# Performance work log

Hardware: AMD Instinct MI355X
Metric: run time of the kernel (lower is better)

## Reference

```python
import jax, jax.numpy as jnp
import numpy as np

B = 32768
NUM_DENSE = 13
PAD_DENSE = 16  # 13 padded up to multiple of 8
T = 26          # number of categorical tables
V = 100000      # cardinality per table
E = 128         # embedding_dim
BOTTOM_DIMS = [512, 256, 128]
TOP_DIMS = [1024, 1024, 512, 256, 1]
N_FEAT = T + 1  # 27 feature vectors entering interaction
PAIR = N_FEAT * (N_FEAT - 1) // 2  # 351
TOP_IN = PAIR + E   # 479
TOP_PAD = 480       # padded to multiple of 8


def _glorot(key, fan_in, fan_out):
    s = np.sqrt(2.0 / (fan_in + fan_out))
    return jax.random.normal(key, (fan_in, fan_out), jnp.float32) * s


def setup_inputs() -> dict:
    key = jax.random.key(0)
    ks = jax.random.split(key, 32)
    inp = {
        "numerical": jax.random.normal(ks[0], (B, NUM_DENSE), jnp.float32),
        "cat_features": jax.random.randint(ks[1], (B, T), 0, V, jnp.int32),
        "emb_tables": jax.random.normal(ks[2], (T, V, E), jnp.float32) * 0.01,
    }
    # bottom MLP: 16 -> 512 -> 256 -> 128 (all relu)
    d_in = PAD_DENSE
    for i, d in enumerate(BOTTOM_DIMS):
        inp[f"bw{i}"] = _glorot(ks[3 + 2 * i], d_in, d)
        inp[f"bb{i}"] = jax.random.normal(ks[4 + 2 * i], (d,), jnp.float32) * np.sqrt(1.0 / d)
        d_in = d
    # top MLP: 480 -> 1024 -> 1024 -> 512 -> 256 -> 1 (relu except last)
    d_in = TOP_PAD
    for i, d in enumerate(TOP_DIMS):
        inp[f"tw{i}"] = _glorot(ks[12 + 2 * i], d_in, d)
        inp[f"tb{i}"] = jax.random.normal(ks[13 + 2 * i], (d,), jnp.float32) * np.sqrt(1.0 / d)
        d_in = d
    return inp


def reference(numerical, cat_features, emb_tables,
              bw0, bb0, bw1, bb1, bw2, bb2,
              tw0, tb0, tw1, tb1, tw2, tb2, tw3, tb3, tw4, tb4):
    b = numerical.shape[0]
    # --- bottom MLP (dense features padded with zeros to 16) ---
    x = jnp.pad(numerical, ((0, 0), (0, PAD_DENSE - NUM_DENSE)))
    for w, bias in ((bw0, bb0), (bw1, bb1), (bw2, bb2)):
        x = jax.nn.relu(x @ w + bias)
    bottom_out = x  # [B, E]
    # --- multi-table embedding gather: emb_tables[t][cat[:, t]] ---
    emb_out = jax.vmap(lambda tab, idx: tab[idx], in_axes=(0, 1), out_axes=1)(
        emb_tables, cat_features)  # [B, T, E]
    # --- dot interaction ---
    feats = jnp.concatenate([bottom_out[:, None, :], emb_out], axis=1)  # [B, 27, E]
    Z = jnp.einsum('bnd,bmd->bnm', feats, feats)  # [B, 27, 27]
    iu, ju = jnp.triu_indices(N_FEAT, k=1)
    pair = Z[:, iu, ju]  # [B, 351]
    x = jnp.concatenate(
        [bottom_out, pair, jnp.zeros((b, TOP_PAD - TOP_IN), feats.dtype)], axis=1)  # [B, 480]
    # --- top MLP (relu except last layer) ---
    tops = ((tw0, tb0), (tw1, tb1), (tw2, tb2), (tw3, tb3), (tw4, tb4))
    for i, (w, bias) in enumerate(tops):
        x = x @ w + bias
        if i < len(tops) - 1:
            x = jax.nn.relu(x)
    return x  # [B, 1] logits
```

## Files before the change

kernel.cpp:

```cpp
#include <hip/hip_runtime.h>

typedef __bf16 bf16;
typedef __bf16 bf16x4 __attribute__((ext_vector_type(4)));
typedef __bf16 bf16x8 __attribute__((ext_vector_type(8)));
typedef float f32x4 __attribute__((ext_vector_type(4)));

#define B_SZ 32768
#define T_CAT 26
#define V_SZ 100000
#define E_SZ 128

__device__ __forceinline__ void gload_lds16(const void* g, void* l) {
    __builtin_amdgcn_global_load_lds(
        (const __attribute__((address_space(1))) void*)g,
        (__attribute__((address_space(3))) void*)l, 16, 0, 0);
}

struct CJob { const float* W; bf16* Wt; int K, N, Kp, blk0, tk; };
struct CJobs { CJob j[7]; };

__global__ __launch_bounds__(256) void convw_all(CJobs js) {
    __shared__ bf16 tile[64][66];
    const int b = blockIdx.x;
    int ji = 0;
#pragma unroll
    for (int k = 1; k < 7; ++k)
        if (b >= js.j[k].blk0) ji = k;
    const CJob J = js.j[ji];
    const int local = b - J.blk0;
    const int tn = local / J.tk;
    const int tkk = local - tn * J.tk;

    const int t = threadIdx.x;
    const int lx = t & 63;
    const int gy = t >> 6;

#pragma unroll
    for (int kk = 0; kk < 16; ++kk) {
        const int k = tkk * 64 + kk * 4 + gy;
        const int n = tn * 64 + lx;
        const float v = (k < J.K) ? J.W[(long)k * J.N + n] : 0.0f;
        tile[lx][kk * 4 + gy] = (bf16)v;
    }
    __syncthreads();
#pragma unroll
    for (int nn = 0; nn < 16; ++nn) {
        const int nloc = nn * 4 + gy;
        const int n = tn * 64 + nloc;
        const int k = tkk * 64 + lx;
        J.Wt[(long)n * J.Kp + k] = tile[nloc][lx];
    }
}

__global__ __launch_bounds__(256) void make_xpad(const float* __restrict__ num,
                                                 bf16* __restrict__ xp) {
    const int idx = blockIdx.x * 256 + threadIdx.x;
    const int b = idx >> 6, c = idx & 63;
    xp[idx] = (bf16)((c < 13) ? num[(long)b * 13 + c] : 0.0f);
}

template <int RELU>
__global__ __launch_bounds__(256) void gemm_bt(const bf16* __restrict__ A,
                                               const bf16* __restrict__ Bt,
                                               const float* __restrict__ bias,
                                               bf16* __restrict__ C,
                                               int M, int N, int K) {
    __shared__ __align__(16) bf16 As[128 * 64];
    __shared__ __align__(16) bf16 Bs[128 * 64];
    const int t = threadIdx.x;
    const int lane = t & 63;
    const int w = t >> 6;
    const int wm = w >> 1, wn = w & 1;
    const long row0 = (long)blockIdx.y * 128;
    const long col0 = (long)blockIdx.x * 128;

    const int srow = t >> 3;
    const int scol = (t & 7) * 8;
    const bf16* Ag = A + (row0 + srow) * (long)K + scol;
    const bf16* Bg = Bt + (col0 + srow) * (long)K + scol;
    bf16* AsB = &As[w * 512];
    bf16* BsB = &Bs[w * 512];

    f32x4 acc[4][4] = {};

    for (int k0 = 0; k0 < K; k0 += 64) {
#pragma unroll
        for (int q = 0; q < 4; ++q) {
            gload_lds16(Ag + (long)q * 32 * K + k0, AsB + q * 2048);
            gload_lds16(Bg + (long)q * 32 * K + k0, BsB + q * 2048);
        }
        __syncthreads();
#pragma unroll
        for (int s = 0; s < 2; ++s) {
            bf16x8 af[4], bv[4];
#pragma unroll
            for (int i = 0; i < 4; ++i)
                af[i] = *(const bf16x8*)&As[(wm * 64 + i * 16 + (lane & 15)) * 64 +
                                            s * 32 + (lane >> 4) * 8];
#pragma unroll
            for (int j = 0; j < 4; ++j)
                bv[j] = *(const bf16x8*)&Bs[(wn * 64 + j * 16 + (lane & 15)) * 64 +
                                            s * 32 + (lane >> 4) * 8];
#pragma unroll
            for (int i = 0; i < 4; ++i)
#pragma unroll
                for (int j = 0; j < 4; ++j)
                    acc[i][j] = __builtin_amdgcn_mfma_f32_16x16x32_bf16(
                        af[i], bv[j], acc[i][j], 0, 0, 0);
        }
        __syncthreads();
    }

    const int r4 = (lane >> 4) * 4;
    const int cn = lane & 15;
#pragma unroll
    for (int j = 0; j < 4; ++j) {
        const long col = col0 + wn * 64 + j * 16 + cn;
        const float bj = bias[col];
#pragma unroll
        for (int i = 0; i < 4; ++i) {
#pragma unroll
            for (int r = 0; r < 4; ++r) {
                const long row = row0 + wm * 64 + i * 16 + r4 + r;
                float v = acc[i][j][r] + bj;
                if (RELU) v = v > 0.0f ? v : 0.0f;
                C[row * (long)N + col] = (bf16)v;
            }
        }
    }
}

template <int RELU>
__global__ __launch_bounds__(512, 2) void gemm256(const bf16* __restrict__ A,
                                                  const bf16* __restrict__ Bt,
                                                  const float* __restrict__ bias,
                                                  bf16* __restrict__ C,
                                                  int M, int N, int K, int nbx) {
    __shared__ __align__(16) bf16 lds[65536];
    const int t = threadIdx.x;
    const int lane = t & 63;
    const int w = t >> 6;
    const int wm = w >> 2, wn = w & 3;

    const int nwg = gridDim.x;
    const int qch = nwg >> 3;
    const int swz = ((int)blockIdx.x & 7) * qch + ((int)blockIdx.x >> 3);
    const int bx = swz % nbx, by = swz / nbx;
    const long row0 = (long)by * 256;
    const long col0 = (long)bx * 256;

    const int NT = K >> 6;

    const int srow = t >> 2;
    const int scol = (t & 3) * 8;
    const bf16* Ag = A + (row0 + srow) * (long)K + scol;
    const bf16* Bg = Bt + (col0 + srow) * (long)K + scol;

#define STG(BUF, MAT, KH, KT)                                              \
    do {                                                                   \
        const bf16* _g = ((MAT) ? Bg : Ag) + (long)(KT)*64 + (KH)*32;      \
        bf16* _l = &lds[(BUF)*32768 + (MAT)*16384 + (KH)*8192 + w * 512];  \
        gload_lds16(_g, _l);                                               \
        gload_lds16(_g + 128 * (long)K, _l + 4096);                        \
    } while (0)

    const int cm = lane & 15;
    const int kc = lane >> 4;
    const int abase = (wm * 128 + cm) * 32 + kc * 8;
    const int bbase = 16384 + (wn * 64 + cm) * 32 + kc * 8;

    bf16x8 bfr[4];
    f32x4 acc[8][4] = {};

#define PH(BUFB, S, IH, LOADB, STAGE, WAIT)                                   \
    do {                                                                      \
        if (LOADB) {                                                          \
            _Pragma("unroll") for (int j = 0; j < 4; ++j)                     \
                bfr[j] = *(const bf16x8*)&lds[(BUFB) + bbase + (S)*8192 + j*512]; \
        }                                                                     \
        bf16x8 af[4];                                                         \
        _Pragma("unroll") for (int i = 0; i < 4; ++i)                         \
            af[i] = *(const bf16x8*)&lds[(BUFB) + abase + (S)*8192 + ((IH)*4+i)*512]; \
        STAGE;                                                                \
        WAIT;                                                                 \
        asm volatile("" ::: "memory");                                       \
        __builtin_amdgcn_s_barrier();                                        \
        asm volatile("s_waitcnt lgkmcnt(0)" ::: "memory");                    \
        __builtin_amdgcn_s_setprio(1);                                       \
        _Pragma("unroll") for (int i = 0; i < 4; ++i)                         \
            _Pragma("unroll") for (int j = 0; j < 4; ++j)                     \
                acc[(IH)*4 + i][j] = __builtin_amdgcn_mfma_f32_16x16x32_bf16( \
                    af[i], bfr[j], acc[(IH)*4 + i][j], 0, 0, 0);              \
        __builtin_amdgcn_s_setprio(0);                                       \
        asm volatile("" ::: "memory");                                       \
        __builtin_amdgcn_s_barrier();                                        \
        asm volatile("" ::: "memory");                                       \
    } while (0)

#define TILE(BUFB, S1, S2, S3, S4, W4)          \
    PH(BUFB, 0, 0, 1, S1, ((void)0));           \
    PH(BUFB, 0, 1, 0, S2, ((void)0));           \
    PH(BUFB, 1, 0, 1, S3, ((void)0));           \
    PH(BUFB, 1, 1, 0, S4, W4)

#define VM6 asm volatile("s_waitcnt vmcnt(6)" ::: "memory")
#define VM0 asm volatile("s_waitcnt vmcnt(0)" ::: "memory")
#define NOP ((void)0)

    STG(0, 1, 0, 0); STG(0, 0, 0, 0); STG(0, 1, 1, 0); STG(0, 0, 1, 0);
    STG(1, 1, 0, 1); STG(1, 0, 0, 1); STG(1, 1, 1, 1);
    VM6;
    __builtin_amdgcn_s_barrier();

    for (int tt = 0; tt + 3 < NT; tt += 2) {
        TILE(0,
             STG(1, 0, 1, tt + 1),
             STG(0, 1, 0, tt + 2),
             STG(0, 0, 0, tt + 2),
             STG(0, 1, 1, tt + 2),
             VM6);
        TILE(32768,
             STG(0, 0, 1, tt + 2),
             STG(1, 1, 0, tt + 3),
             STG(1, 0, 0, tt + 3),
             STG(1, 1, 1, tt + 3),
             VM6);
    }
    TILE(0, STG(1, 0, 1, NT - 1), NOP, NOP, NOP, VM0);
    TILE(32768, NOP, NOP, NOP, NOP, NOP);

#undef STG
#undef PH
#undef TILE
#undef VM6
#undef VM0
#undef NOP

    const int r4 = kc * 4;
#pragma unroll
    for (int j = 0; j < 4; ++j) {
        const long col = col0 + wn * 64 + j * 16 + cm;
        const float bj = bias[col];
#pragma unroll
        for (int i = 0; i < 8; ++i) {
#pragma unroll
            for (int r = 0; r < 4; ++r) {
                const long row = row0 + wm * 128 + i * 16 + r4 + r;
                float v = acc[i][j][r] + bj;
                if (RELU) v = v > 0.0f ? v : 0.0f;
                C[row * (long)N + col] = (bf16)v;
            }
        }
    }
}

__global__ __launch_bounds__(256) void interact_k(const float* __restrict__ emb,
                                                  const int* __restrict__ cat,
                                                  const bf16* __restrict__ bottom,
                                                  bf16* __restrict__ top_in) {
    __shared__ float gram[4][32 * 32];
    __shared__ __align__(16) bf16 rowbuf[4][512];
    const int t = threadIdx.x;
    const int lane = t & 63;
    const int w = t >> 6;
    const long s = (long)blockIdx.x * 4 + w;

    const int rl = lane & 15;
    const int kg = lane >> 4;

    bf16x8 f[2][4];
#pragma unroll
    for (int i = 0; i < 2; ++i) {
        const int r = i * 16 + rl;
        const float* rowp = nullptr;
        if (r >= 1 && r <= 26) {
            const int idx = cat[s * T_CAT + (r - 1)];
            rowp = emb + ((long)(r - 1) * V_SZ + idx) * E_SZ;
        }
#pragma unroll
        for (int ks = 0; ks < 4; ++ks) {
            const int c = ks * 32 + kg * 8;
            bf16x8 v = {};
            if (r == 0) {
                v = *(const bf16x8*)(bottom + s * 128 + c);
            } else if (r <= 26) {
                const float4 v0 = *(const float4*)(rowp + c);
                const float4 v1 = *(const float4*)(rowp + c + 4);
                v[0]=(bf16)v0.x; v[1]=(bf16)v0.y; v[2]=(bf16)v0.z; v[3]=(bf16)v0.w;
                v[4]=(bf16)v1.x; v[5]=(bf16)v1.y; v[6]=(bf16)v1.z; v[7]=(bf16)v1.w;
            }
            f[i][ks] = v;
        }
    }

    f32x4 a00 = {}, a01 = {}, a11 = {};
#pragma unroll
    for (int ks = 0; ks < 4; ++ks) {
        a00 = __builtin_amdgcn_mfma_f32_16x16x32_bf16(f[0][ks], f[0][ks], a00, 0, 0, 0);
        a01 = __builtin_amdgcn_mfma_f32_16x16x32_bf16(f[0][ks], f[1][ks], a01, 0, 0, 0);
        a11 = __builtin_amdgcn_mfma_f32_16x16x32_bf16(f[1][ks], f[1][ks], a11, 0, 0, 0);
    }

    const int r4 = kg * 4;
#pragma unroll
    for (int r = 0; r < 4; ++r) {
        gram[w][(r4 + r) * 32 + rl]           = a00[r];
        gram[w][(r4 + r) * 32 + 16 + rl]      = a01[r];
        gram[w][(16 + r4 + r) * 32 + 16 + rl] = a11[r];
    }
    asm volatile("s_waitcnt lgkmcnt(0)" ::: "memory");
    __builtin_amdgcn_sched_barrier(0);

    if (lane < 16)
        ((bf16x8*)&rowbuf[w][0])[lane] = ((const bf16x8*)(bottom + s * 128))[lane];
    for (int p = lane; p < 351; p += 64) {
        int i = 0, b = 0;
        while (b + (26 - i) <= p) { b += 26 - i; ++i; }
        const int j = p - b + i + 1;
        rowbuf[w][128 + p] = (bf16)gram[w][i * 32 + j];
    }
    if (lane >= 31) rowbuf[w][448 + lane] = (bf16)0.0f;
    asm volatile("s_waitcnt lgkmcnt(0)" ::: "memory");
    __builtin_amdgcn_sched_barrier(0);

    *(bf16x8*)(top_in + s * 512 + lane * 8) = *(const bf16x8*)&rowbuf[w][lane * 8];
}

__global__ __launch_bounds__(256) void gemv_final(const bf16* __restrict__ A,
                                                  const float* __restrict__ w4,
                                                  const float* __restrict__ b4,
                                                  float* __restrict__ out) {
    const int t = threadIdx.x;
    const int lane = t & 63;
    const int w = t >> 6;
    const long m = (long)blockIdx.x * 4 + w;
    const bf16x4 v = *(const bf16x4*)(A + m * 256 + lane * 4);
    const float4 wv = *(const float4*)(w4 + lane * 4);
    float sum = (float)v[0] * wv.x + (float)v[1] * wv.y + (float)v[2] * wv.z +
                (float)v[3] * wv.w;
#pragma unroll
    for (int off = 32; off > 0; off >>= 1) sum += __shfl_down(sum, off);
    if (lane == 0) out[m] = sum + b4[0];
}

extern "C" void kernel_launch(void* const* d_in, const int* in_sizes, int n_in,
                              void* d_out, int out_size, void* d_ws, size_t ws_size,
                              hipStream_t stream) {
    const float* numerical = (const float*)d_in[0];
    const int*   cat       = (const int*)d_in[1];
    const float* emb       = (const float*)d_in[2];
    const float* bw0 = (const float*)d_in[3];
    const float* bb0 = (const float*)d_in[4];
    const float* bw1 = (const float*)d_in[5];
    const float* bb1 = (const float*)d_in[6];
    const float* bw2 = (const float*)d_in[7];
    const float* bb2 = (const float*)d_in[8];
    const float* tw0 = (const float*)d_in[9];
    const float* tb0 = (const float*)d_in[10];
    const float* tw1 = (const float*)d_in[11];
    const float* tb1 = (const float*)d_in[12];
    const float* tw2 = (const float*)d_in[13];
    const float* tb2 = (const float*)d_in[14];
    const float* tw3 = (const float*)d_in[15];
    const float* tb3 = (const float*)d_in[16];
    const float* tw4 = (const float*)d_in[17];
    const float* tb4 = (const float*)d_in[18];
    float* out = (float*)d_out;

    char* ws = (char*)d_ws;
    size_t off = 0;
    auto alloc = [&](size_t bytes) {
        char* p = ws + off;
        off += (bytes + 255) & ~(size_t)255;
        return p;
    };
    bf16* wt0b = (bf16*)alloc((size_t)512 * 64 * 2);
    bf16* wt1b = (bf16*)alloc((size_t)256 * 512 * 2);
    bf16* wt2b = (bf16*)alloc((size_t)128 * 256 * 2);
    bf16* wt0t = (bf16*)alloc((size_t)1024 * 512 * 2);
    bf16* wt1t = (bf16*)alloc((size_t)1024 * 1024 * 2);
    bf16* wt2t = (bf16*)alloc((size_t)512 * 1024 * 2);
    bf16* wt3t = (bf16*)alloc((size_t)256 * 512 * 2);
    bf16* xpad = (bf16*)alloc((size_t)B_SZ * 64 * 2);
    bf16* h0   = (bf16*)alloc((size_t)B_SZ * 512 * 2);
    bf16* h1   = (bf16*)alloc((size_t)B_SZ * 256 * 2);
    bf16* bot  = (bf16*)alloc((size_t)B_SZ * 128 * 2);
    bf16* t0   = (bf16*)alloc((size_t)B_SZ * 1024 * 2);
    bf16* t1   = (bf16*)alloc((size_t)B_SZ * 1024 * 2);
    bf16* top_in = h0;
    bf16* t2 = t0;
    bf16* t3 = t1;

    CJobs js;
    js.j[0] = {bw0, wt0b, 16, 512, 64, 0, 1};
    js.j[1] = {bw1, wt1b, 512, 256, 512, 8, 8};
    js.j[2] = {bw2, wt2b, 256, 128, 256, 40, 4};
    js.j[3] = {tw0, wt0t, 480, 1024, 512, 48, 8};
    js.j[4] = {tw1, wt1t, 1024, 1024, 1024, 176, 16};
    js.j[5] = {tw2, wt2t, 1024, 512, 1024, 432, 16};
    js.j[6] = {tw3, wt3t, 512, 256, 512, 560, 8};
    convw_all<<<592, 256, 0, stream>>>(js);

    make_xpad<<<(B_SZ * 64) / 256, 256, 0, stream>>>(numerical, xpad);

    gemm_bt<1><<<dim3(4, 256), 256, 0, stream>>>(xpad, wt0b, bb0, h0, B_SZ, 512, 64);
    gemm256<1><<<dim3(128), 512, 0, stream>>>(h0, wt1b, bb1, h1, B_SZ, 256, 512, 1);
    gemm_bt<1><<<dim3(1, 256), 256, 0, stream>>>(h1, wt2b, bb2, bot, B_SZ, 128, 256);

    interact_k<<<B_SZ / 4, 256, 0, stream>>>(emb, cat, bot, top_in);

    gemm256<1><<<dim3(4 * 128), 512, 0, stream>>>(top_in, wt0t, tb0, t0, B_SZ, 1024, 512, 4);
    gemm256<1><<<dim3(4 * 128), 512, 0, stream>>>(t0, wt1t, tb1, t1, B_SZ, 1024, 1024, 4);
    gemm256<1><<<dim3(2 * 128), 512, 0, stream>>>(t1, wt2t, tb2, t2, B_SZ, 512, 1024, 2);
    gemm256<1><<<dim3(128), 512, 0, stream>>>(t2, wt3t, tb3, t3, B_SZ, 256, 512, 1);

    gemv_final<<<B_SZ / 4, 256, 0, stream>>>(t3, tw4, tb4, out);
}
```

Baseline: 388.6 us.

## Swizzle GEMM LDS layout, use triu lookup table, switch small GEMMs to gemm_bt

Applies an XOR swizzle to the 16-byte column chunks that gemm256 stages into LDS and reads back, to cut LDS bank conflicts on the MFMA fragment loads. The interaction kernel replaces its per-element while-loop triangular index search with a compile-time lookup table. The N=256 GEMMs in the bottom and top MLPs now launch gemm_bt with more blocks instead of gemm256 with only 128 workgroups, which should fill more compute units. The swizzle has to match on both the store and load side, and the table adds a constant-memory read.

```diff
diff --git a/kernel.cpp b/kernel.cpp
--- a/kernel.cpp
+++ b/kernel.cpp
@@ -15,6 +15,17 @@
         (const __attribute__((address_space(1))) void*)g,
         (__attribute__((address_space(3))) void*)l, 16, 0, 0);
 }
+
+struct TriuLut { unsigned short v[352]; };
+static constexpr TriuLut makeTriu() {
+    TriuLut l{};
+    int p = 0;
+    for (int i = 0; i < 27; ++i)
+        for (int j = i + 1; j < 27; ++j) l.v[p++] = (unsigned short)(i * 32 + j);
+    l.v[351] = 0;
+    return l;
+}
+__device__ constexpr TriuLut kTriu = makeTriu();
 
 struct CJob { const float* W; bf16* Wt; int K, N, Kp, blk0, tk; };
 struct CJobs { CJob j[7]; };
@@ -152,9 +163,9 @@
     const int NT = K >> 6;
 
     const int srow = t >> 2;
-    const int scol = (t & 3) * 8;
-    const bf16* Ag = A + (row0 + srow) * (long)K + scol;
-    const bf16* Bg = Bt + (col0 + srow) * (long)K + scol;
+    const int gsl = (t & 3) ^ ((srow >> 1) & 3);
+    const bf16* Ag = A + (row0 + srow) * (long)K + gsl * 8;
+    const bf16* Bg = Bt + (col0 + srow) * (long)K + gsl * 8;
 
 #define STG(BUF, MAT, KH, KT)                                              \
     do {                                                                   \
@@ -166,8 +177,9 @@
 
     const int cm = lane & 15;
     const int kc = lane >> 4;
-    const int abase = (wm * 128 + cm) * 32 + kc * 8;
-    const int bbase = 16384 + (wn * 64 + cm) * 32 + kc * 8;
+    const int kswz = (kc ^ ((cm >> 1) & 3)) * 8;
+    const int abase = (wm * 128 + cm) * 32 + kswz;
+    const int bbase = 16384 + (wn * 64 + cm) * 32 + kswz;
 
     bf16x8 bfr[4];
     f32x4 acc[8][4] = {};
@@ -313,11 +325,10 @@
 
     if (lane < 16)
         ((bf16x8*)&rowbuf[w][0])[lane] = ((const bf16x8*)(bottom + s * 128))[lane];
-    for (int p = lane; p < 351; p += 64) {
-        int i = 0, b = 0;
-        while (b + (26 - i) <= p) { b += 26 - i; ++i; }
-        const int j = p - b + i + 1;
-        rowbuf[w][128 + p] = (bf16)gram[w][i * 32 + j];
+#pragma unroll
+    for (int q = 0; q < 6; ++q) {
+        const int p = q * 64 + lane;
+        if (p < 351) rowbuf[w][128 + p] = (bf16)gram[w][kTriu.v[p]];
     }
     if (lane >= 31) rowbuf[w][448 + lane] = (bf16)0.0f;
     asm volatile("s_waitcnt lgkmcnt(0)" ::: "memory");
@@ -404,7 +415,7 @@
     make_xpad<<<(B_SZ * 64) / 256, 256, 0, stream>>>(numerical, xpad);
 
     gemm_bt<1><<<dim3(4, 256), 256, 0, stream>>>(xpad, wt0b, bb0, h0, B_SZ, 512, 64);
-    gemm256<1><<<dim3(128), 512, 0, stream>>>(h0, wt1b, bb1, h1, B_SZ, 256, 512, 1);
+    gemm_bt<1><<<dim3(2, 256), 256, 0, stream>>>(h0, wt1b, bb1, h1, B_SZ, 256, 512);
     gemm_bt<1><<<dim3(1, 256), 256, 0, stream>>>(h1, wt2b, bb2, bot, B_SZ, 128, 256);
 
     interact_k<<<B_SZ / 4, 256, 0, stream>>>(emb, cat, bot, top_in);
@@ -412,7 +423,7 @@
     gemm256<1><<<dim3(4 * 128), 512, 0, stream>>>(top_in, wt0t, tb0, t0, B_SZ, 1024, 512, 4);
     gemm256<1><<<dim3(4 * 128), 512, 0, stream>>>(t0, wt1t, tb1, t1, B_SZ, 1024, 1024, 4);
     gemm256<1><<<dim3(2 * 128), 512, 0, stream>>>(t1, wt2t, tb2, t2, B_SZ, 512, 1024, 2);
-    gemm256<1><<<dim3(128), 512, 0, stream>>>(t2, wt3t, tb3, t3, B_SZ, 256, 512, 1);
+    gemm_bt<1><<<dim3(2, 256), 256, 0, stream>>>(t2, wt3t, tb3, t3, B_SZ, 256, 512);
 
     gemv_final<<<B_SZ / 4, 256, 0, stream>>>(t3, tw4, tb4, out);
 }
```

Result: faster. 373.9 us (-3.8%).
